# Kernel optimization log

Hardware: AMD Instinct MI355X
Metric: run time of the kernel (lower is better)

## Reference

```python
import jax, jax.numpy as jnp
import numpy as np

N_SRC = 2_000_000   # coords at feat_depth (fine level)
N_TGT = 1_000_000   # coords at feat_depth-1 (coarse level)
E = 8_000_000       # neighbor edges from get_neighbours
C = 32              # feature channels


def setup_inputs() -> dict:
    key = jax.random.key(0)
    k1, k2, k3, k4 = jax.random.split(key, 4)
    feat = jax.random.normal(k1, (N_SRC, C), dtype=jnp.float32)
    src_ids = jax.random.randint(k2, (E,), 0, N_SRC)
    tgt_ids = jax.random.randint(k3, (E,), 0, N_TGT)
    ntypes = jax.random.randint(k4, (E, 3), -1, 27).astype(jnp.int32)
    return {"feat": feat, "src_ids": src_ids, "tgt_ids": tgt_ids,
            "ntypes": ntypes, "n_tgt": N_TGT}


def reference(feat, src_ids, tgt_ids, ntypes, n_tgt):
    # p_masks = torch.all(ntypes >= 0, dim=1)
    p_mask = jnp.all(ntypes >= 0, axis=1)                  # [E] bool
    # Route masked-out edges to a dummy segment (index n_tgt) instead of
    # boolean-filtering, keeping shapes static for jit.
    seg = jnp.where(p_mask, tgt_ids, n_tgt)                # [E]
    gathered = feat[src_ids]                               # [E, C] irregular gather
    sums = jax.ops.segment_sum(gathered, seg, num_segments=n_tgt + 1)[:n_tgt]
    counts = jax.ops.segment_sum(jnp.ones((seg.shape[0],), feat.dtype), seg,
                                 num_segments=n_tgt + 1)[:n_tgt]
    # scatter_mean: empty segments yield 0 (torch_scatter semantics)
    out = jnp.where(counts[:, None] > 0, sums / jnp.maximum(counts[:, None], 1), 0.0)
    return out  # feat_depth - 1 is a trivial python int, omitted
```

## Files before the change

### kernel.cpp

```cpp
#include <hip/hip_runtime.h>


#define CCH 32
#define BSH 10
#define BKT 1024
#define CAP 8960
#define BIN_TILE 8192
typedef unsigned int u32;
typedef float f32x4 __attribute__((ext_vector_type(4)));

__global__ __launch_bounds__(256) void init_bcur_kernel(u32* __restrict__ bcur,
                                                        int NB) {
  int i = blockIdx.x * 256 + threadIdx.x;
  if (i < NB) bcur[i] = (u32)i * (u32)CAP;
}

__global__ __launch_bounds__(1024) void bin_fixed_kernel(
    const int* __restrict__ src_ids, const int* __restrict__ tgt_ids,
    const int* __restrict__ ntypes, u32* __restrict__ bcur,
    u32* __restrict__ pairs, int E, int NB) {
  __shared__ unsigned short s_b[BIN_TILE];
  __shared__ u32 s_pw[BIN_TILE];
  __shared__ u32 s_cnt[2048];
  __shared__ u32 s_base[2048];
  const long long base = (long long)blockIdx.x * BIN_TILE;

  for (int j = threadIdx.x; j < 2048; j += 1024) s_cnt[j] = 0;
  __syncthreads();

  for (int k = 0; k < BIN_TILE / 1024; ++k) {
    const int i = threadIdx.x + k * 1024;
    const long long e = base + i;
    unsigned short bb = 0xFFFFu;
    u32 pw = 0;
    if (e < E) {
      const long long eb = 3LL * e;
      const int n0 = __builtin_nontemporal_load(&ntypes[eb]);
      const int n1 = __builtin_nontemporal_load(&ntypes[eb + 1]);
      const int n2 = __builtin_nontemporal_load(&ntypes[eb + 2]);
      if ((n0 | n1 | n2) >= 0) {
        const u32 t = (u32)__builtin_nontemporal_load(&tgt_ids[e]);
        const u32 s = (u32)__builtin_nontemporal_load(&src_ids[e]);
        bb = (unsigned short)(t >> BSH);
        pw = (s << BSH) | (t & (BKT - 1u));
        atomicAdd(&s_cnt[bb], 1u);
      }
    }
    s_b[i] = bb;
    s_pw[i] = pw;
  }
  __syncthreads();

  for (int j = threadIdx.x; j < NB; j += 1024) {
    const u32 c = s_cnt[j];
    s_base[j] = c ? atomicAdd(&bcur[j], c) : 0u;
    s_cnt[j] = 0;
  }
  __syncthreads();

  for (int k = 0; k < BIN_TILE / 1024; ++k) {
    const int i = threadIdx.x + k * 1024;
    const unsigned short bb = s_b[i];
    if (bb != 0xFFFFu) {
      const u32 loc = atomicAdd(&s_cnt[bb], 1u);
      const u32 slot = s_base[bb] + loc;
      if (slot < ((u32)bb + 1u) * (u32)CAP) pairs[slot] = s_pw[i];
    }
  }
}

__global__ __launch_bounds__(1024, 8) void sort_gather_kernel(
    const float* __restrict__ feat, const u32* __restrict__ pairs,
    const u32* __restrict__ bcur, float* __restrict__ out, int n_tgt) {
  __shared__ u32 s_pw[CAP];
  __shared__ u32 s_srt[CAP];
  __shared__ u32 s_cnt[BKT];
  __shared__ u32 s_off[BKT];
  const int b = blockIdx.x;
  const u32 wbeg = (u32)b * (u32)CAP;
  u32 fill = bcur[b] - wbeg;
  if (fill > (u32)CAP) fill = (u32)CAP;

  for (u32 i = threadIdx.x; i < fill; i += 1024)
    s_pw[i] = __builtin_nontemporal_load(&pairs[wbeg + i]);
  s_cnt[threadIdx.x] = 0;
  __syncthreads();
  for (u32 i = threadIdx.x; i < fill; i += 1024)
    atomicAdd(&s_cnt[s_pw[i] & (BKT - 1u)], 1u);
  __syncthreads();

  const u32 v = s_cnt[threadIdx.x];
  s_off[threadIdx.x] = v;
  __syncthreads();
  for (int d = 1; d < BKT; d <<= 1) {
    const u32 add = (threadIdx.x >= (unsigned)d) ? s_off[threadIdx.x - d] : 0u;
    __syncthreads();
    s_off[threadIdx.x] += add;
    __syncthreads();
  }
  s_cnt[threadIdx.x] = s_off[threadIdx.x] - v;
  __syncthreads();
  for (u32 i = threadIdx.x; i < fill; i += 1024) {
    const u32 pw = s_pw[i];
    const u32 loc = atomicAdd(&s_cnt[pw & (BKT - 1u)], 1u);
    s_srt[loc] = pw >> BSH;
  }
  __syncthreads();

  const int grp = threadIdx.x >> 3;
  const int lane = threadIdx.x & 7;
  const int l4 = lane * 4;
  const long long t0 = (long long)b << BSH;
  for (int r = grp; r < BKT; r += 128) {
    const long long t = t0 + r;
    if (t >= n_tgt) break;
    const u32 beg = r ? s_off[r - 1] : 0u;
    const u32 n = s_off[r] - beg;
    f32x4 acc = {0.f, 0.f, 0.f, 0.f};
    for (u32 c = 0; c < n; c += 8) {
      const u32 m = n - c;
      u32 idx[8];
#pragma unroll
      for (int k = 0; k < 8; ++k)
        idx[k] = s_srt[beg + c + ((u32)k < m ? (u32)k : 0u)];
      f32x4 vv[8];
#pragma unroll
      for (int k = 0; k < 8; ++k)
        vv[k] = *reinterpret_cast<const f32x4*>(feat +
                                                (long long)idx[k] * CCH + l4);
#pragma unroll
      for (int k = 0; k < 8; ++k) {
        const float w = ((u32)k < m) ? 1.0f : 0.0f;
        acc += vv[k] * w;
      }
    }
    const float inv = n ? 1.0f / (float)n : 0.0f;
    acc *= inv;
    *reinterpret_cast<f32x4*>(out + t * CCH + l4) = acc;
  }
}


__global__ __launch_bounds__(256) void scatter_accum_kernel(
    const float* __restrict__ feat, const int* __restrict__ src_ids,
    const int* __restrict__ tgt_ids, const int* __restrict__ ntypes,
    float* __restrict__ sums, u32* __restrict__ counts,
    long long total_threads) {
  long long tid = (long long)blockIdx.x * blockDim.x + threadIdx.x;
  if (tid >= total_threads) return;
  const int e = (int)(tid >> 3);
  const int g = (int)(tid & 7);
  const long long eb = 3LL * e;
  if ((ntypes[eb] | ntypes[eb + 1] | ntypes[eb + 2]) < 0) return;
  const int s = src_ids[e];
  const int t = tgt_ids[e];
  const float4 v =
      *reinterpret_cast<const float4*>(feat + (long long)s * CCH + g * 4);
  float* dst = sums + (long long)t * CCH + g * 4;
  atomicAdd(dst + 0, v.x);
  atomicAdd(dst + 1, v.y);
  atomicAdd(dst + 2, v.z);
  atomicAdd(dst + 3, v.w);
  if (g == 0) atomicAdd(counts + t, 1u);
}

__global__ __launch_bounds__(256) void finalize_kernel(
    float* __restrict__ out, const u32* __restrict__ counts, int total_vec4) {
  int tid = blockIdx.x * blockDim.x + threadIdx.x;
  if (tid >= total_vec4) return;
  const int t = tid >> 3;
  const u32 cnt = counts[t];
  float4* p = reinterpret_cast<float4*>(out) + tid;
  float4 v = *p;
  const float inv = (cnt > 0u) ? (1.0f / (float)cnt) : 0.0f;
  v.x *= inv; v.y *= inv; v.z *= inv; v.w *= inv;
  *p = v;
}


extern "C" void kernel_launch(void* const* d_in, const int* in_sizes, int n_in,
                              void* d_out, int out_size, void* d_ws,
                              size_t ws_size, hipStream_t stream) {
  const float* feat    = (const float*)d_in[0];
  const int*   src_ids = (const int*)d_in[1];
  const int*   tgt_ids = (const int*)d_in[2];
  const int*   ntypes  = (const int*)d_in[3];
  const int E     = in_sizes[1];
  const int n_src = in_sizes[0] / CCH;
  const int n_tgt = out_size / CCH;

  const int NB = (n_tgt + BKT - 1) >> BSH;

  const size_t need = ((size_t)NB * CAP + NB) * sizeof(u32);
  const long long mean_fill = ((long long)E * BKT + n_tgt - 1) / n_tgt;
  const bool shapes_ok =
      NB <= 2048 && n_src <= (1 << 21) && mean_fill <= 8192;

  if (ws_size >= need && shapes_ok) {
    u32* pairs = (u32*)d_ws;
    u32* bcur  = pairs + (size_t)NB * CAP;

    init_bcur_kernel<<<(NB + 255) / 256, 256, 0, stream>>>(bcur, NB);
    const int bblocks = (E + BIN_TILE - 1) / BIN_TILE;
    bin_fixed_kernel<<<bblocks, 1024, 0, stream>>>(src_ids, tgt_ids, ntypes,
                                                   bcur, pairs, E, NB);
    sort_gather_kernel<<<NB, 1024, 0, stream>>>(feat, pairs, bcur,
                                                (float*)d_out, n_tgt);
  } else {
    float* sums   = (float*)d_out;
    u32*   counts = (u32*)d_ws;
    hipMemsetAsync(d_out, 0, (size_t)out_size * sizeof(float), stream);
    hipMemsetAsync(d_ws, 0, (size_t)n_tgt * sizeof(u32), stream);
    const long long total_threads = (long long)E * 8;
    const long long nblocks = (total_threads + 255) / 256;
    scatter_accum_kernel<<<(dim3)((unsigned int)nblocks), 256, 0, stream>>>(
        feat, src_ids, tgt_ids, ntypes, sums, counts, total_threads);
    const int total_vec4 = n_tgt * 8;
    finalize_kernel<<<(total_vec4 + 255) / 256, 256, 0, stream>>>(
        sums, counts, total_vec4);
  }
}
```

Baseline: 268.6 us.

## Use wavefront-shuffle prefix scan, smaller bin blocks, and nontemporal output stores

Swaps the 10-step shared-memory Hillis-Steele scan in the sort-gather kernel for a two-level wavefront shuffle scan. This cuts the number of block-wide barriers from about twenty to a few. The binning kernel drops to 512 threads and 4096-edge tiles, which gives more blocks and more global atomics on the bucket cursors. Output writes become nontemporal stores to avoid polluting the cache.

New measurement: 278.5 us. 3.7% more time.

```diff
diff --git a/kernel.cpp b/kernel.cpp
--- a/kernel.cpp
+++ b/kernel.cpp
@@ -5,7 +5,8 @@
 #define BSH 10
 #define BKT 1024
 #define CAP 8960
-#define BIN_TILE 8192
+#define BIN_THREADS 512
+#define BIN_TILE 4096
 typedef unsigned int u32;
 typedef float f32x4 __attribute__((ext_vector_type(4)));
 
@@ -15,7 +16,7 @@
   if (i < NB) bcur[i] = (u32)i * (u32)CAP;
 }
 
-__global__ __launch_bounds__(1024) void bin_fixed_kernel(
+__global__ __launch_bounds__(BIN_THREADS) void bin_fixed_kernel(
     const int* __restrict__ src_ids, const int* __restrict__ tgt_ids,
     const int* __restrict__ ntypes, u32* __restrict__ bcur,
     u32* __restrict__ pairs, int E, int NB) {
@@ -25,11 +26,11 @@
   __shared__ u32 s_base[2048];
   const long long base = (long long)blockIdx.x * BIN_TILE;
 
-  for (int j = threadIdx.x; j < 2048; j += 1024) s_cnt[j] = 0;
-  __syncthreads();
-
-  for (int k = 0; k < BIN_TILE / 1024; ++k) {
-    const int i = threadIdx.x + k * 1024;
+  for (int j = threadIdx.x; j < 2048; j += BIN_THREADS) s_cnt[j] = 0;
+  __syncthreads();
+
+  for (int k = 0; k < BIN_TILE / BIN_THREADS; ++k) {
+    const int i = threadIdx.x + k * BIN_THREADS;
     const long long e = base + i;
     unsigned short bb = 0xFFFFu;
     u32 pw = 0;
@@ -51,15 +52,15 @@
   }
   __syncthreads();
 
-  for (int j = threadIdx.x; j < NB; j += 1024) {
+  for (int j = threadIdx.x; j < NB; j += BIN_THREADS) {
     const u32 c = s_cnt[j];
     s_base[j] = c ? atomicAdd(&bcur[j], c) : 0u;
     s_cnt[j] = 0;
   }
   __syncthreads();
 
-  for (int k = 0; k < BIN_TILE / 1024; ++k) {
-    const int i = threadIdx.x + k * 1024;
+  for (int k = 0; k < BIN_TILE / BIN_THREADS; ++k) {
+    const int i = threadIdx.x + k * BIN_THREADS;
     const unsigned short bb = s_b[i];
     if (bb != 0xFFFFu) {
       const u32 loc = atomicAdd(&s_cnt[bb], 1u);
@@ -76,6 +77,7 @@
   __shared__ u32 s_srt[CAP];
   __shared__ u32 s_cnt[BKT];
   __shared__ u32 s_off[BKT];
+  __shared__ u32 s_wt[16];
   const int b = blockIdx.x;
   const u32 wbeg = (u32)b * (u32)CAP;
   u32 fill = bcur[b] - wbeg;
@@ -89,17 +91,32 @@
     atomicAdd(&s_cnt[s_pw[i] & (BKT - 1u)], 1u);
   __syncthreads();
 
+  const u32 lane = threadIdx.x & 63u;
+  const u32 wid = threadIdx.x >> 6;
   const u32 v = s_cnt[threadIdx.x];
-  s_off[threadIdx.x] = v;
-  __syncthreads();
-  for (int d = 1; d < BKT; d <<= 1) {
-    const u32 add = (threadIdx.x >= (unsigned)d) ? s_off[threadIdx.x - d] : 0u;
-    __syncthreads();
-    s_off[threadIdx.x] += add;
-    __syncthreads();
-  }
-  s_cnt[threadIdx.x] = s_off[threadIdx.x] - v;
-  __syncthreads();
+  u32 x = v;
+#pragma unroll
+  for (int d = 1; d < 64; d <<= 1) {
+    const u32 y = __shfl_up(x, d, 64);
+    if (lane >= (u32)d) x += y;
+  }
+  if (lane == 63u) s_wt[wid] = x;
+  __syncthreads();
+  if (wid == 0) {
+    u32 w = (lane < 16u) ? s_wt[lane] : 0u;
+#pragma unroll
+    for (int d = 1; d < 16; d <<= 1) {
+      const u32 y = __shfl_up(w, d, 64);
+      if (lane >= (u32)d) w += y;
+    }
+    if (lane < 16u) s_wt[lane] = w;
+  }
+  __syncthreads();
+  const u32 incl = x + (wid ? s_wt[wid - 1] : 0u);
+  s_off[threadIdx.x] = incl;
+  s_cnt[threadIdx.x] = incl - v;
+  __syncthreads();
+
   for (u32 i = threadIdx.x; i < fill; i += 1024) {
     const u32 pw = s_pw[i];
     const u32 loc = atomicAdd(&s_cnt[pw & (BKT - 1u)], 1u);
@@ -108,8 +125,7 @@
   __syncthreads();
 
   const int grp = threadIdx.x >> 3;
-  const int lane = threadIdx.x & 7;
-  const int l4 = lane * 4;
+  const int l4 = (threadIdx.x & 7) * 4;
   const long long t0 = (long long)b << BSH;
   for (int r = grp; r < BKT; r += 128) {
     const long long t = t0 + r;
@@ -136,7 +152,8 @@
     }
     const float inv = n ? 1.0f / (float)n : 0.0f;
     acc *= inv;
-    *reinterpret_cast<f32x4*>(out + t * CCH + l4) = acc;
+    __builtin_nontemporal_store(acc,
+                                reinterpret_cast<f32x4*>(out + t * CCH + l4));
   }
 }
 
@@ -202,8 +219,8 @@
 
     init_bcur_kernel<<<(NB + 255) / 256, 256, 0, stream>>>(bcur, NB);
     const int bblocks = (E + BIN_TILE - 1) / BIN_TILE;
-    bin_fixed_kernel<<<bblocks, 1024, 0, stream>>>(src_ids, tgt_ids, ntypes,
-                                                   bcur, pairs, E, NB);
+    bin_fixed_kernel<<<bblocks, BIN_THREADS, 0, stream>>>(
+        src_ids, tgt_ids, ntypes, bcur, pairs, E, NB);
     sort_gather_kernel<<<NB, 1024, 0, stream>>>(feat, pairs, bcur,
                                                 (float*)d_out, n_tgt);
   } else {
```
